# Kernel optimization log

Measured on AMD Instinct MI355X. Metric: run time of the kernel, lower is better.

## Reference

```python
import jax, jax.numpy as jnp
import numpy as np

B, F0, D = 2048, 40, 32
LAYER0, LAYER1 = 128, 128  # layer_size=(128,128), split_half=True -> field_nums=[40,64]


def setup_inputs() -> dict:
    key = jax.random.key(0)
    k1, k2, k3 = jax.random.split(key, 3)
    x = jax.random.normal(k1, (B, F0, D), dtype=jnp.float32)
    # TF conv1d filters: [1, F_prev*F0, size]; we store them reshaped [F0, F_prev_fields, size]
    # Layer 0: F_prev = F0 = 40 -> W0 flattened index m = i*F0 + j, i over x0 fields, j over hidden fields
    W0 = jax.random.normal(k2, (F0, F0, LAYER0), dtype=jnp.float32) * 0.05
    b0 = jnp.zeros((LAYER0,), dtype=jnp.float32)
    # Layer 1: F_prev = LAYER0 // 2 = 64 (split_half)
    W1 = jax.random.normal(k3, (F0, LAYER0 // 2, LAYER1), dtype=jnp.float32) * 0.05
    b1 = jnp.zeros((LAYER1,), dtype=jnp.float32)
    return {"x": x, "W0": W0, "b0": b0, "W1": W1, "b1": b1}


def reference(x, W0, b0, W1, b1):
    # CIN layer 0: outer product x0 (x) x0 over fields per embedding dim, then 1x1 conv + bias + relu
    # TF flattens dot_result as index i*F_prev + j, matching W0[i, j, s].
    h0 = jax.nn.relu(jnp.einsum('bid,bjd,ijs->bsd', x, x, W0) + b0[None, :, None])  # (B, 128, D)
    half = LAYER0 // 2
    next_hidden, direct0 = h0[:, :half, :], h0[:, half:, :]  # split_half
    # CIN layer 1 (last layer): all feature maps go to direct connect
    direct1 = jax.nn.relu(
        jnp.einsum('bid,bjd,ijs->bsd', x, next_hidden, W1) + b1[None, :, None]
    )  # (B, 128, D)
    result = jnp.concatenate([direct0, direct1], axis=1)  # (B, 192, D)
    return jnp.sum(result, axis=-1)  # (B, 192)
```

## Files before the change

kernel.cpp:

```cpp
#include <hip/hip_runtime.h>
#include <stdint.h>


typedef __attribute__((ext_vector_type(8))) _Float16 half8;
typedef __attribute__((ext_vector_type(2))) _Float16 half2v;
typedef __attribute__((ext_vector_type(16))) float f32x16;

#define T0 30
#define T1 80
#define WBUF 8192

__host__ __device__ constexpr int ic0_of(int t) {
    return (t < 2) ? t : (t < 6) ? (t - 2) : (t < 12) ? (t - 6)
         : (t < 20) ? (t - 12) : (t - 20);
}
__host__ __device__ constexpr int jc0_of(int t) {
    return (t < 2) ? 0 : (t < 6) ? 1 : (t < 12) ? 2 : (t < 20) ? 3 : 4;
}

__device__ __forceinline__ unsigned short f2h(float f) {
    return __builtin_bit_cast(unsigned short, (_Float16)f);
}
__device__ __forceinline__ void gl_lds16(const unsigned short* g, unsigned short* l) {
    __builtin_amdgcn_global_load_lds(
        (const __attribute__((address_space(1))) unsigned int*)g,
        (__attribute__((address_space(3))) unsigned int*)l,
        16, 0, 0);
}
__device__ __forceinline__ uint4 avmul(half2v xs, uint4 jv) {
    uint4 r;
    r.x = __builtin_bit_cast(unsigned int, (half2v)(xs * __builtin_bit_cast(half2v, jv.x)));
    r.y = __builtin_bit_cast(unsigned int, (half2v)(xs * __builtin_bit_cast(half2v, jv.y)));
    r.z = __builtin_bit_cast(unsigned int, (half2v)(xs * __builtin_bit_cast(half2v, jv.z)));
    r.w = __builtin_bit_cast(unsigned int, (half2v)(xs * __builtin_bit_cast(half2v, jv.w)));
    return r;
}

__global__ void permute_w_both(const float* __restrict__ W0, const float* __restrict__ W1,
                               unsigned short* __restrict__ Wp0, unsigned short* __restrict__ Wp1)
{
    const int t = blockIdx.x;
    const int tid = threadIdx.x;
    unsigned short outv[16];
    unsigned short* dst;
    if (t < T0) {
        const int ic = ic0_of(t), jc = jc0_of(t);
        #pragma unroll
        for (int q = 0; q < 16; ++q) {
            int pos  = tid * 16 + q;
            int e    = pos & 7, lane = (pos >> 3) & 63;
            int kh   = (pos >> 9) & 1, sq = pos >> 10;
            int s    = sq * 32 + (lane & 31);
            int i    = ic * 4 + kh * 2 + (lane >> 5);
            int j    = jc * 8 + e;
            float v = 0.0f;
            if (i < j)       v = W0[((size_t)(i * 40 + j)) * 128 + s]
                               + W0[((size_t)(j * 40 + i)) * 128 + s];
            else if (i == j) v = W0[((size_t)(i * 40 + i)) * 128 + s];
            outv[q] = f2h(v);
        }
        dst = Wp0 + (size_t)t * 4096 + tid * 16;
    } else {
        const int tt = t - T0;
        const int jc = tt / 10, ic = tt % 10;
        #pragma unroll
        for (int q = 0; q < 16; ++q) {
            int pos  = tid * 16 + q;
            int e    = pos & 7, lane = (pos >> 3) & 63;
            int kh   = (pos >> 9) & 1, sq = pos >> 10;
            int s    = sq * 32 + (lane & 31);
            int i    = ic * 4 + kh * 2 + (lane >> 5);
            int j    = jc * 8 + e;
            outv[q] = f2h(W1[((size_t)(i * 64 + j)) * 128 + s]);
        }
        dst = Wp1 + (size_t)tt * 4096 + tid * 16;
    }
    *(uint4*)dst       = *(const uint4*)outv;
    *(uint4*)(dst + 8) = *(const uint4*)(outv + 8);
}

template<int T, int PHASE>
__device__ __forceinline__ void gemm_phase(
    const unsigned short* __restrict__ Wp,
    const unsigned short* __restrict__ Jl,
    int jstride,
    const unsigned int xk[2][10],
    unsigned short* Wb,
    f32x16 acc[2], int tid)
{
    const int lane = tid & 63;
    const int wv = tid >> 6;
    const int rt = wv >> 2;
    const int sq = wv & 3;
    const int c31 = lane & 31;

    const unsigned short* jbase = Jl + (rt * 64 + c31) * jstride;

    const unsigned short* brd = Wb + sq * 1024 + lane * 8;
    const unsigned short* gsrc = Wp + tid * 8;
    unsigned short* ldst = Wb + tid * 8;

    auto stage = [&](int k) {
        gl_lds16(gsrc + (size_t)k * WBUF, ldst + (k % 3) * WBUF);
    };

    constexpr int NP = T / 2;
    stage(0);
    stage(1);

    uint4 jv0, jv1;
    #pragma unroll
    for (int p = 0; p < NP; ++p) {
        if (p == NP - 1) asm volatile("s_waitcnt vmcnt(0)" ::: "memory");
        else             asm volatile("s_waitcnt vmcnt(1)" ::: "memory");
        __builtin_amdgcn_sched_barrier(0);
        __builtin_amdgcn_s_barrier();
        __builtin_amdgcn_sched_barrier(0);
        if (p + 2 < NP) stage(p + 2);
        __builtin_amdgcn_sched_barrier(0);

        const unsigned short* bper = brd + (p % 3) * WBUF;
        #pragma unroll
        for (int u = 0; u < 2; ++u) {
            const int t  = p * 2 + u;
            const int ic = (PHASE == 0) ? ic0_of(t) : (t % 10);
            const int jc = (PHASE == 0) ? jc0_of(t) : (t / 10);
            const bool rl = (t == 0) ||
                (jc != ((PHASE == 0) ? jc0_of(t - 1) : ((t - 1) / 10)));
            if (rl) {
                jv0 = *(const uint4*)(jbase + jc * 8);
                jv1 = *(const uint4*)(jbase + 32 * jstride + jc * 8);
            }
            __builtin_amdgcn_s_setprio(1);
            #pragma unroll
            for (int kh = 0; kh < 2; ++kh) {
                uint4 bvv = *(const uint4*)(bper + u * 4096 + kh * 512);
                half2v xp = __builtin_bit_cast(half2v, xk[kh][ic]);
                half2v x0 = {xp[0], xp[0]};
                half2v x1 = {xp[1], xp[1]};
                acc[0] = __builtin_amdgcn_mfma_f32_32x32x16_f16(
                    __builtin_bit_cast(half8, avmul(x0, jv0)),
                    __builtin_bit_cast(half8, bvv), acc[0], 0, 0, 0);
                acc[1] = __builtin_amdgcn_mfma_f32_32x32x16_f16(
                    __builtin_bit_cast(half8, avmul(x1, jv1)),
                    __builtin_bit_cast(half8, bvv), acc[1], 0, 0, 0);
            }
            __builtin_amdgcn_s_setprio(0);
        }
    }
}

__global__ __launch_bounds__(1024, 4)
void fused_two_layer(const float* __restrict__ x,
                     const unsigned short* __restrict__ W0p,
                     const float* __restrict__ b0,
                     const unsigned short* __restrict__ W1p,
                     const float* __restrict__ b1,
                     float* __restrict__ out)
{
    __shared__ __align__(16) unsigned short Xl[256 * 40];
    __shared__ __align__(16) unsigned short NH[256 * 72];
    __shared__ __align__(16) unsigned short Wb[3 * WBUF];

    const int tid  = threadIdx.x;
    const int lane = tid & 63;
    const int wv   = tid >> 6;
    const int rt   = wv >> 2;
    const int sq   = wv & 3;
    const int c31  = lane & 31;
    const int hb   = lane >> 5;

    const float* xblk = x + (size_t)blockIdx.x * (8 * 40 * 32);
    #pragma unroll
    for (int k = 0; k < 10; ++k) {
        int f = 1024 * k + tid;
        int bl = f / 1280, rem = f - bl * 1280;
        int i = rem >> 5, d = rem & 31;
        Xl[(bl * 32 + d) * 40 + i] = f2h(xblk[f]);
    }
    __syncthreads();

    unsigned int xk[2][10];
    {
        const unsigned short* xr0 = Xl + (rt * 64 + c31) * 40;
        const unsigned short* xr1 = xr0 + 32 * 40;
        #pragma unroll
        for (int ic = 0; ic < 10; ++ic)
            #pragma unroll
            for (int kh = 0; kh < 2; ++kh) {
                unsigned int u0 = xr0[ic * 4 + kh * 2 + hb];
                unsigned int u1 = xr1[ic * 4 + kh * 2 + hb];
                xk[kh][ic] = u0 | (u1 << 16);
            }
    }

    f32x16 acc[2];
    #pragma unroll
    for (int rtt = 0; rtt < 2; ++rtt)
        #pragma unroll
        for (int rg = 0; rg < 16; ++rg) acc[rtt][rg] = 0.f;

    gemm_phase<T0, 0>(W0p, Xl, 40, xk, Wb, acc, tid);

    {
        float bs = b0[sq * 32 + c31];
        if (sq < 2) {
            #pragma unroll
            for (int rtt = 0; rtt < 2; ++rtt)
                #pragma unroll
                for (int rg = 0; rg < 16; ++rg) {
                    int row = rt * 64 + rtt * 32 + (rg & 3) + 8 * (rg >> 2) + 4 * hb;
                    NH[row * 72 + sq * 32 + c31] =
                        f2h(fmaxf(acc[rtt][rg] + bs, 0.0f));
                }
        } else {
            #pragma unroll
            for (int rtt = 0; rtt < 2; ++rtt) {
                float s = 0.f;
                #pragma unroll
                for (int rg = 0; rg < 16; ++rg)
                    s += fmaxf(acc[rtt][rg] + bs, 0.0f);
                s += __shfl_xor(s, 32, 64);
                int bb = blockIdx.x * 8 + rt * 2 + rtt;
                if (lane < 32)
                    out[(size_t)bb * 192 + (sq - 2) * 32 + c31] = s;
            }
        }
    }
    __syncthreads();

    #pragma unroll
    for (int rtt = 0; rtt < 2; ++rtt)
        #pragma unroll
        for (int rg = 0; rg < 16; ++rg) acc[rtt][rg] = 0.f;

    gemm_phase<T1, 1>(W1p, NH, 72, xk, Wb, acc, tid);

    {
        float bs = b1[sq * 32 + c31];
        #pragma unroll
        for (int rtt = 0; rtt < 2; ++rtt) {
            float s = 0.f;
            #pragma unroll
            for (int rg = 0; rg < 16; ++rg)
                s += fmaxf(acc[rtt][rg] + bs, 0.0f);
            s += __shfl_xor(s, 32, 64);
            int bb = blockIdx.x * 8 + rt * 2 + rtt;
            if (lane < 32)
                out[(size_t)bb * 192 + 64 + sq * 32 + c31] = s;
        }
    }
}

extern "C" void kernel_launch(void* const* d_in, const int* in_sizes, int n_in,
                              void* d_out, int out_size, void* d_ws, size_t ws_size,
                              hipStream_t stream) {
    const float* x  = (const float*)d_in[0];
    const float* W0 = (const float*)d_in[1];
    const float* b0 = (const float*)d_in[2];
    const float* W1 = (const float*)d_in[3];
    const float* b1 = (const float*)d_in[4];
    float* out = (float*)d_out;

    unsigned short* W0p = (unsigned short*)d_ws;
    unsigned short* W1p = (unsigned short*)((char*)d_ws + T0 * 4096 * 2);

    permute_w_both<<<T0 + T1, 256, 0, stream>>>(W0, W1, W0p, W1p);
    fused_two_layer<<<256, 1024, 0, stream>>>(x, W0p, b0, W1p, b1, out);
}
```

Measured before the change: 120.0 us.

## Software-pipeline LDS B-operand reads and A-operand construction in the MFMA loop

Restructures the inner GEMM loop into a flat sequence of half-steps. The B fragment is read from LDS two MFMA pairs ahead, and the scaled A operand (x times hidden) is built one step ahead, so LDS latency and VALU multiplies overlap with MFMA execution. The global-to-LDS weight staging now waits for all outstanding loads (vmcnt(0)) each step instead of leaving one in flight. That may reduce the effective prefetch depth and adds live registers under tight launch bounds.

```diff
diff --git a/kernel.cpp b/kernel.cpp
--- a/kernel.cpp
+++ b/kernel.cpp
@@ -15,7 +15,7 @@
          : (t < 20) ? (t - 12) : (t - 20);
 }
 __host__ __device__ constexpr int jc0_of(int t) {
-    return (t < 2) ? 0 : (t < 6) ? 1 : (t < 12) ? 2 : (t < 20) ? 3 : 4;
+    return (t < 0) ? 0 : (t < 2) ? 0 : (t < 6) ? 1 : (t < 12) ? 2 : (t < 20) ? 3 : 4;
 }
 
 __device__ __forceinline__ unsigned short f2h(float f) {
@@ -94,58 +94,82 @@
     const int sq = wv & 3;
     const int c31 = lane & 31;
 
-    const unsigned short* jbase = Jl + (rt * 64 + c31) * jstride;
-
+    const unsigned short* jbase0 = Jl + (rt * 64 + c31) * jstride;
+    const unsigned short* jbase1 = jbase0 + 32 * jstride;
     const unsigned short* brd = Wb + sq * 1024 + lane * 8;
     const unsigned short* gsrc = Wp + tid * 8;
     unsigned short* ldst = Wb + tid * 8;
 
-    auto stage = [&](int k) {
-        gl_lds16(gsrc + (size_t)k * WBUF, ldst + (k % 3) * WBUF);
-    };
-
-    constexpr int NP = T / 2;
-    stage(0);
-    stage(1);
+    constexpr int NP  = T / 2;
+    constexpr int NHT = T * 2;
+
+    gl_lds16(gsrc, ldst);
+    gl_lds16(gsrc + (size_t)WBUF, ldst + WBUF);
+    asm volatile("s_waitcnt vmcnt(0)" ::: "memory");
+    __builtin_amdgcn_sched_barrier(0);
+    __builtin_amdgcn_s_barrier();
+    __builtin_amdgcn_sched_barrier(0);
+    gl_lds16(gsrc + (size_t)2 * WBUF, ldst + 2 * WBUF);
 
     uint4 jv0, jv1;
+    {
+        const int jc0 = (PHASE == 0) ? jc0_of(0) : 0;
+        jv0 = *(const uint4*)(jbase0 + jc0 * 8);
+        jv1 = *(const uint4*)(jbase1 + jc0 * 8);
+    }
+    uint4 bvp[3];
+    bvp[0] = *(const uint4*)(brd + 0 * 512);
+    bvp[1] = *(const uint4*)(brd + 1 * 512);
+    uint4 avp[2][2];
+    {
+        const int ic0 = (PHASE == 0) ? ic0_of(0) : 0;
+        half2v xp = __builtin_bit_cast(half2v, xk[0][ic0]);
+        half2v x0 = {xp[0], xp[0]}, x1 = {xp[1], xp[1]};
+        avp[0][0] = avmul(x0, jv0);
+        avp[0][1] = avmul(x1, jv1);
+    }
+
     #pragma unroll
     for (int p = 0; p < NP; ++p) {
-        if (p == NP - 1) asm volatile("s_waitcnt vmcnt(0)" ::: "memory");
-        else             asm volatile("s_waitcnt vmcnt(1)" ::: "memory");
-        __builtin_amdgcn_sched_barrier(0);
-        __builtin_amdgcn_s_barrier();
-        __builtin_amdgcn_sched_barrier(0);
-        if (p + 2 < NP) stage(p + 2);
-        __builtin_amdgcn_sched_barrier(0);
-
-        const unsigned short* bper = brd + (p % 3) * WBUF;
-        #pragma unroll
-        for (int u = 0; u < 2; ++u) {
-            const int t  = p * 2 + u;
-            const int ic = (PHASE == 0) ? ic0_of(t) : (t % 10);
-            const int jc = (PHASE == 0) ? jc0_of(t) : (t / 10);
-            const bool rl = (t == 0) ||
-                (jc != ((PHASE == 0) ? jc0_of(t - 1) : ((t - 1) / 10)));
-            if (rl) {
-                jv0 = *(const uint4*)(jbase + jc * 8);
-                jv1 = *(const uint4*)(jbase + 32 * jstride + jc * 8);
-            }
+        if (p > 0) {
+            asm volatile("s_waitcnt vmcnt(0)" ::: "memory");
+            __builtin_amdgcn_sched_barrier(0);
+            __builtin_amdgcn_s_barrier();
+            __builtin_amdgcn_sched_barrier(0);
+            if (p + 2 < NP)
+                gl_lds16(gsrc + (size_t)(p + 2) * WBUF, ldst + ((p + 2) % 3) * WBUF);
+        }
+        #pragma unroll
+        for (int u2 = 0; u2 < 4; ++u2) {
+            const int h = p * 4 + u2;
             __builtin_amdgcn_s_setprio(1);
-            #pragma unroll
-            for (int kh = 0; kh < 2; ++kh) {
-                uint4 bvv = *(const uint4*)(bper + u * 4096 + kh * 512);
-                half2v xp = __builtin_bit_cast(half2v, xk[kh][ic]);
-                half2v x0 = {xp[0], xp[0]};
-                half2v x1 = {xp[1], xp[1]};
-                acc[0] = __builtin_amdgcn_mfma_f32_32x32x16_f16(
-                    __builtin_bit_cast(half8, avmul(x0, jv0)),
-                    __builtin_bit_cast(half8, bvv), acc[0], 0, 0, 0);
-                acc[1] = __builtin_amdgcn_mfma_f32_32x32x16_f16(
-                    __builtin_bit_cast(half8, avmul(x1, jv1)),
-                    __builtin_bit_cast(half8, bvv), acc[1], 0, 0, 0);
-            }
+            acc[0] = __builtin_amdgcn_mfma_f32_32x32x16_f16(
+                __builtin_bit_cast(half8, avp[h & 1][0]),
+                __builtin_bit_cast(half8, bvp[h % 3]), acc[0], 0, 0, 0);
+            acc[1] = __builtin_amdgcn_mfma_f32_32x32x16_f16(
+                __builtin_bit_cast(half8, avp[h & 1][1]),
+                __builtin_bit_cast(half8, bvp[h % 3]), acc[1], 0, 0, 0);
             __builtin_amdgcn_s_setprio(0);
+            if (h + 2 < NHT) {
+                const int t2 = (h + 2) >> 1, kh2 = (h + 2) & 1;
+                const int p2 = t2 >> 1,     u2b = t2 & 1;
+                bvp[(h + 2) % 3] = *(const uint4*)
+                    (brd + (p2 % 3) * WBUF + u2b * 4096 + kh2 * 512);
+            }
+            if (h + 1 < NHT) {
+                const int t1 = (h + 1) >> 1, kh1 = (h + 1) & 1;
+                const int icn = (PHASE == 0) ? ic0_of(t1) : (t1 % 10);
+                const int jcn = (PHASE == 0) ? jc0_of(t1) : (t1 / 10);
+                const int jcp = (PHASE == 0) ? jc0_of(t1 - 1) : ((t1 - 1) / 10);
+                if (kh1 == 0 && jcn != jcp) {
+                    jv0 = *(const uint4*)(jbase0 + jcn * 8);
+                    jv1 = *(const uint4*)(jbase1 + jcn * 8);
+                }
+                half2v xp = __builtin_bit_cast(half2v, xk[kh1][icn]);
+                half2v x0 = {xp[0], xp[0]}, x1 = {xp[1], xp[1]};
+                avp[(h + 1) & 1][0] = avmul(x0, jv0);
+                avp[(h + 1) & 1][1] = avmul(x1, jv1);
+            }
         }
     }
 }
```

Measured after the change: 117.9 us. Within noise of the previous version (-1.7%).

## Halve block to 512 threads with 2x2 MFMA tiles per wave

Applied to the files above, without the earlier changes.

Each wave now computes two 32-column output tiles instead of one, so every A operand built from x*hidden products feeds two MFMAs, and the block shrinks from 16 to 8 waves. Each thread stages two weight chunks per pipeline step to keep the LDS fill the same, and the epilogues are remapped to the new wave layout. The aim is to cut the redundant avmul work and LDS reads of the A side per MFMA. The cost is twice the accumulator registers and fewer waves per block to hide latency.

```diff
diff --git a/kernel.cpp b/kernel.cpp
--- a/kernel.cpp
+++ b/kernel.cpp
@@ -86,22 +86,23 @@
     int jstride,
     const unsigned int xk[2][10],
     unsigned short* Wb,
-    f32x16 acc[2], int tid)
+    f32x16 acc[2][2], int tid)
 {
     const int lane = tid & 63;
     const int wv = tid >> 6;
-    const int rt = wv >> 2;
-    const int sq = wv & 3;
+    const int rt = wv >> 1;
+    const int sh = wv & 1;
     const int c31 = lane & 31;
 
-    const unsigned short* jbase = Jl + (rt * 64 + c31) * jstride;
-
-    const unsigned short* brd = Wb + sq * 1024 + lane * 8;
+    const unsigned short* jbase0 = Jl + (rt * 64 + c31) * jstride;
+    const unsigned short* jbase1 = jbase0 + 32 * jstride;
+    const unsigned short* brd = Wb + sh * 2048 + lane * 8;
     const unsigned short* gsrc = Wp + tid * 8;
     unsigned short* ldst = Wb + tid * 8;
 
     auto stage = [&](int k) {
-        gl_lds16(gsrc + (size_t)k * WBUF, ldst + (k % 3) * WBUF);
+        gl_lds16(gsrc + (size_t)k * WBUF,        ldst + (k % 3) * WBUF);
+        gl_lds16(gsrc + (size_t)k * WBUF + 4096, ldst + (k % 3) * WBUF + 4096);
     };
 
     constexpr int NP = T / 2;
@@ -112,7 +113,7 @@
     #pragma unroll
     for (int p = 0; p < NP; ++p) {
         if (p == NP - 1) asm volatile("s_waitcnt vmcnt(0)" ::: "memory");
-        else             asm volatile("s_waitcnt vmcnt(1)" ::: "memory");
+        else             asm volatile("s_waitcnt vmcnt(2)" ::: "memory");
         __builtin_amdgcn_sched_barrier(0);
         __builtin_amdgcn_s_barrier();
         __builtin_amdgcn_sched_barrier(0);
@@ -128,29 +129,38 @@
             const bool rl = (t == 0) ||
                 (jc != ((PHASE == 0) ? jc0_of(t - 1) : ((t - 1) / 10)));
             if (rl) {
-                jv0 = *(const uint4*)(jbase + jc * 8);
-                jv1 = *(const uint4*)(jbase + 32 * jstride + jc * 8);
+                jv0 = *(const uint4*)(jbase0 + jc * 8);
+                jv1 = *(const uint4*)(jbase1 + jc * 8);
             }
             __builtin_amdgcn_s_setprio(1);
             #pragma unroll
             for (int kh = 0; kh < 2; ++kh) {
-                uint4 bvv = *(const uint4*)(bper + u * 4096 + kh * 512);
+                uint4 bv0 = *(const uint4*)(bper + u * 4096 + kh * 512);
+                uint4 bv1 = *(const uint4*)(bper + u * 4096 + kh * 512 + 1024);
                 half2v xp = __builtin_bit_cast(half2v, xk[kh][ic]);
                 half2v x0 = {xp[0], xp[0]};
                 half2v x1 = {xp[1], xp[1]};
-                acc[0] = __builtin_amdgcn_mfma_f32_32x32x16_f16(
-                    __builtin_bit_cast(half8, avmul(x0, jv0)),
-                    __builtin_bit_cast(half8, bvv), acc[0], 0, 0, 0);
-                acc[1] = __builtin_amdgcn_mfma_f32_32x32x16_f16(
-                    __builtin_bit_cast(half8, avmul(x1, jv1)),
-                    __builtin_bit_cast(half8, bvv), acc[1], 0, 0, 0);
+                uint4 av0 = avmul(x0, jv0);
+                uint4 av1 = avmul(x1, jv1);
+                acc[0][0] = __builtin_amdgcn_mfma_f32_32x32x16_f16(
+                    __builtin_bit_cast(half8, av0),
+                    __builtin_bit_cast(half8, bv0), acc[0][0], 0, 0, 0);
+                acc[0][1] = __builtin_amdgcn_mfma_f32_32x32x16_f16(
+                    __builtin_bit_cast(half8, av0),
+                    __builtin_bit_cast(half8, bv1), acc[0][1], 0, 0, 0);
+                acc[1][0] = __builtin_amdgcn_mfma_f32_32x32x16_f16(
+                    __builtin_bit_cast(half8, av1),
+                    __builtin_bit_cast(half8, bv0), acc[1][0], 0, 0, 0);
+                acc[1][1] = __builtin_amdgcn_mfma_f32_32x32x16_f16(
+                    __builtin_bit_cast(half8, av1),
+                    __builtin_bit_cast(half8, bv1), acc[1][1], 0, 0, 0);
             }
             __builtin_amdgcn_s_setprio(0);
         }
     }
 }
 
-__global__ __launch_bounds__(1024, 4)
+__global__ __launch_bounds__(512, 2)
 void fused_two_layer(const float* __restrict__ x,
                      const unsigned short* __restrict__ W0p,
                      const float* __restrict__ b0,
@@ -165,15 +175,15 @@
     const int tid  = threadIdx.x;
     const int lane = tid & 63;
     const int wv   = tid >> 6;
-    const int rt   = wv >> 2;
-    const int sq   = wv & 3;
+    const int rt   = wv >> 1;
+    const int sh   = wv & 1;
     const int c31  = lane & 31;
     const int hb   = lane >> 5;
 
     const float* xblk = x + (size_t)blockIdx.x * (8 * 40 * 32);
     #pragma unroll
-    for (int k = 0; k < 10; ++k) {
-        int f = 1024 * k + tid;
+    for (int k = 0; k < 20; ++k) {
+        int f = 512 * k + tid;
         int bl = f / 1280, rem = f - bl * 1280;
         int i = rem >> 5, d = rem & 31;
         Xl[(bl * 32 + d) * 40 + i] = f2h(xblk[f]);
@@ -194,60 +204,72 @@
             }
     }
 
-    f32x16 acc[2];
-    #pragma unroll
-    for (int rtt = 0; rtt < 2; ++rtt)
-        #pragma unroll
-        for (int rg = 0; rg < 16; ++rg) acc[rtt][rg] = 0.f;
+    f32x16 acc[2][2];
+    #pragma unroll
+    for (int a = 0; a < 2; ++a)
+        #pragma unroll
+        for (int b = 0; b < 2; ++b)
+            #pragma unroll
+            for (int rg = 0; rg < 16; ++rg) acc[a][b][rg] = 0.f;
 
     gemm_phase<T0, 0>(W0p, Xl, 40, xk, Wb, acc, tid);
 
     {
-        float bs = b0[sq * 32 + c31];
-        if (sq < 2) {
+        float bs[2] = { b0[sh * 64 + c31], b0[sh * 64 + 32 + c31] };
+        if (sh == 0) {
             #pragma unroll
             for (int rtt = 0; rtt < 2; ++rtt)
                 #pragma unroll
-                for (int rg = 0; rg < 16; ++rg) {
-                    int row = rt * 64 + rtt * 32 + (rg & 3) + 8 * (rg >> 2) + 4 * hb;
-                    NH[row * 72 + sq * 32 + c31] =
-                        f2h(fmaxf(acc[rtt][rg] + bs, 0.0f));
+                for (int ct = 0; ct < 2; ++ct)
+                    #pragma unroll
+                    for (int rg = 0; rg < 16; ++rg) {
+                        int row = rt * 64 + rtt * 32 + (rg & 3) + 8 * (rg >> 2) + 4 * hb;
+                        NH[row * 72 + ct * 32 + c31] =
+                            f2h(fmaxf(acc[rtt][ct][rg] + bs[ct], 0.0f));
+                    }
+        } else {
+            #pragma unroll
+            for (int rtt = 0; rtt < 2; ++rtt) {
+                int bb = blockIdx.x * 8 + rt * 2 + rtt;
+                #pragma unroll
+                for (int ct = 0; ct < 2; ++ct) {
+                    float s = 0.f;
+                    #pragma unroll
+                    for (int rg = 0; rg < 16; ++rg)
+                        s += fmaxf(acc[rtt][ct][rg] + bs[ct], 0.0f);
+                    s += __shfl_xor(s, 32, 64);
+                    if (lane < 32)
+                        out[(size_t)bb * 192 + ct * 32 + c31] = s;
                 }
-        } else {
-            #pragma unroll
-            for (int rtt = 0; rtt < 2; ++rtt) {
+            }
+        }
+    }
+    __syncthreads();
+
+    #pragma unroll
+    for (int a = 0; a < 2; ++a)
+        #pragma unroll
+        for (int b = 0; b < 2; ++b)
+            #pragma unroll
+            for (int rg = 0; rg < 16; ++rg) acc[a][b][rg] = 0.f;
+
+    gemm_phase<T1, 1>(W1p, NH, 72, xk, Wb, acc, tid);
+
+    {
+        float bs[2] = { b1[sh * 64 + c31], b1[sh * 64 + 32 + c31] };
+        #pragma unroll
+        for (int rtt = 0; rtt < 2; ++rtt) {
+            int bb = blockIdx.x * 8 + rt * 2 + rtt;
+            #pragma unroll
+            for (int ct = 0; ct < 2; ++ct) {
                 float s = 0.f;
                 #pragma unroll
                 for (int rg = 0; rg < 16; ++rg)
-                    s += fmaxf(acc[rtt][rg] + bs, 0.0f);
+                    s += fmaxf(acc[rtt][ct][rg] + bs[ct], 0.0f);
                 s += __shfl_xor(s, 32, 64);
-                int bb = blockIdx.x * 8 + rt * 2 + rtt;
                 if (lane < 32)
-                    out[(size_t)bb * 192 + (sq - 2) * 32 + c31] = s;
-            }
-        }
-    }
-    __syncthreads();
-
-    #pragma unroll
-    for (int rtt = 0; rtt < 2; ++rtt)
-        #pragma unroll
-        for (int rg = 0; rg < 16; ++rg) acc[rtt][rg] = 0.f;
-
-    gemm_phase<T1, 1>(W1p, NH, 72, xk, Wb, acc, tid);
-
-    {
-        float bs = b1[sq * 32 + c31];
-        #pragma unroll
-        for (int rtt = 0; rtt < 2; ++rtt) {
-            float s = 0.f;
-            #pragma unroll
-            for (int rg = 0; rg < 16; ++rg)
-                s += fmaxf(acc[rtt][rg] + bs, 0.0f);
-            s += __shfl_xor(s, 32, 64);
-            int bb = blockIdx.x * 8 + rt * 2 + rtt;
-            if (lane < 32)
-                out[(size_t)bb * 192 + 64 + sq * 32 + c31] = s;
+                    out[(size_t)bb * 192 + 64 + sh * 64 + ct * 32 + c31] = s;
+            }
         }
     }
 }
@@ -266,5 +288,5 @@
     unsigned short* W1p = (unsigned short*)((char*)d_ws + T0 * 4096 * 2);
 
     permute_w_both<<<T0 + T1, 256, 0, stream>>>(W0, W1, W0p, W1p);
-    fused_two_layer<<<256, 1024, 0, stream>>>(x, W0p, b0, W1p, b1, out);
-}
+    fused_two_layer<<<256, 512, 0, stream>>>(x, W0p, b0, W1p, b1, out);
+}
```

New measurement: 118.8 us. Within noise of the previous version (-1.0%).

## Halve block size to 512 threads and stage one weight tile per step

Applied to the files above, without the earlier changes.

Each block now handles 4 batch rows with 512 threads instead of 8 rows with 1024, and the launch doubles the grid to 512 blocks. The weight pipeline stages one 4096-element tile per barrier step instead of two, so there are twice as many barrier steps. The NH row stride drops from 72 to 68, and shared memory per block shrinks so more blocks can be resident per CU. The aim is better CU occupancy and load balance across more blocks, at the cost of more barriers and each block re-fetching the same weights from global memory.

```diff
diff --git a/kernel.cpp b/kernel.cpp
--- a/kernel.cpp
+++ b/kernel.cpp
@@ -8,7 +8,8 @@
 
 #define T0 30
 #define T1 80
-#define WBUF 8192
+#define TBUF 4096
+#define NHS 68
 
 __host__ __device__ constexpr int ic0_of(int t) {
     return (t < 2) ? t : (t < 6) ? (t - 2) : (t < 12) ? (t - 6)
@@ -94,63 +95,58 @@
     const int sq = wv & 3;
     const int c31 = lane & 31;
 
-    const unsigned short* jbase = Jl + (rt * 64 + c31) * jstride;
-
+    const unsigned short* jbase0 = Jl + (rt * 64 + c31) * jstride;
+    const unsigned short* jbase1 = jbase0 + 32 * jstride;
     const unsigned short* brd = Wb + sq * 1024 + lane * 8;
     const unsigned short* gsrc = Wp + tid * 8;
     unsigned short* ldst = Wb + tid * 8;
 
     auto stage = [&](int k) {
-        gl_lds16(gsrc + (size_t)k * WBUF, ldst + (k % 3) * WBUF);
+        gl_lds16(gsrc + (size_t)k * TBUF, ldst + (k % 3) * TBUF);
     };
 
-    constexpr int NP = T / 2;
     stage(0);
     stage(1);
 
     uint4 jv0, jv1;
     #pragma unroll
-    for (int p = 0; p < NP; ++p) {
-        if (p == NP - 1) asm volatile("s_waitcnt vmcnt(0)" ::: "memory");
-        else             asm volatile("s_waitcnt vmcnt(1)" ::: "memory");
+    for (int p = 0; p < T; ++p) {
+        if (p == T - 1) asm volatile("s_waitcnt vmcnt(0)" ::: "memory");
+        else            asm volatile("s_waitcnt vmcnt(1)" ::: "memory");
         __builtin_amdgcn_sched_barrier(0);
         __builtin_amdgcn_s_barrier();
         __builtin_amdgcn_sched_barrier(0);
-        if (p + 2 < NP) stage(p + 2);
+        if (p + 2 < T) stage(p + 2);
         __builtin_amdgcn_sched_barrier(0);
 
-        const unsigned short* bper = brd + (p % 3) * WBUF;
-        #pragma unroll
-        for (int u = 0; u < 2; ++u) {
-            const int t  = p * 2 + u;
-            const int ic = (PHASE == 0) ? ic0_of(t) : (t % 10);
-            const int jc = (PHASE == 0) ? jc0_of(t) : (t / 10);
-            const bool rl = (t == 0) ||
-                (jc != ((PHASE == 0) ? jc0_of(t - 1) : ((t - 1) / 10)));
-            if (rl) {
-                jv0 = *(const uint4*)(jbase + jc * 8);
-                jv1 = *(const uint4*)(jbase + 32 * jstride + jc * 8);
-            }
-            __builtin_amdgcn_s_setprio(1);
-            #pragma unroll
-            for (int kh = 0; kh < 2; ++kh) {
-                uint4 bvv = *(const uint4*)(bper + u * 4096 + kh * 512);
-                half2v xp = __builtin_bit_cast(half2v, xk[kh][ic]);
-                half2v x0 = {xp[0], xp[0]};
-                half2v x1 = {xp[1], xp[1]};
-                acc[0] = __builtin_amdgcn_mfma_f32_32x32x16_f16(
-                    __builtin_bit_cast(half8, avmul(x0, jv0)),
-                    __builtin_bit_cast(half8, bvv), acc[0], 0, 0, 0);
-                acc[1] = __builtin_amdgcn_mfma_f32_32x32x16_f16(
-                    __builtin_bit_cast(half8, avmul(x1, jv1)),
-                    __builtin_bit_cast(half8, bvv), acc[1], 0, 0, 0);
-            }
-            __builtin_amdgcn_s_setprio(0);
-        }
-    }
-}
-
-__global__ __launch_bounds__(1024, 4)
+        const int ic = (PHASE == 0) ? ic0_of(p) : (p % 10);
+        const int jc = (PHASE == 0) ? jc0_of(p) : (p / 10);
+        const bool rl = (p == 0) ||
+            (jc != ((PHASE == 0) ? jc0_of(p - 1) : ((p - 1) / 10)));
+        if (rl) {
+            jv0 = *(const uint4*)(jbase0 + jc * 8);
+            jv1 = *(const uint4*)(jbase1 + jc * 8);
+        }
+        const unsigned short* bper = brd + (p % 3) * TBUF;
+        __builtin_amdgcn_s_setprio(1);
+        #pragma unroll
+        for (int kh = 0; kh < 2; ++kh) {
+            uint4 bvv = *(const uint4*)(bper + kh * 512);
+            half2v xp = __builtin_bit_cast(half2v, xk[kh][ic]);
+            half2v x0 = {xp[0], xp[0]};
+            half2v x1 = {xp[1], xp[1]};
+            acc[0] = __builtin_amdgcn_mfma_f32_32x32x16_f16(
+                __builtin_bit_cast(half8, avmul(x0, jv0)),
+                __builtin_bit_cast(half8, bvv), acc[0], 0, 0, 0);
+            acc[1] = __builtin_amdgcn_mfma_f32_32x32x16_f16(
+                __builtin_bit_cast(half8, avmul(x1, jv1)),
+                __builtin_bit_cast(half8, bvv), acc[1], 0, 0, 0);
+        }
+        __builtin_amdgcn_s_setprio(0);
+    }
+}
+
+__global__ __launch_bounds__(512, 4)
 void fused_two_layer(const float* __restrict__ x,
                      const unsigned short* __restrict__ W0p,
                      const float* __restrict__ b0,
@@ -158,9 +154,9 @@
                      const float* __restrict__ b1,
                      float* __restrict__ out)
 {
-    __shared__ __align__(16) unsigned short Xl[256 * 40];
-    __shared__ __align__(16) unsigned short NH[256 * 72];
-    __shared__ __align__(16) unsigned short Wb[3 * WBUF];
+    __shared__ __align__(16) unsigned short Xl[128 * 40];
+    __shared__ __align__(16) unsigned short NH[128 * NHS];
+    __shared__ __align__(16) unsigned short Wb[3 * TBUF];
 
     const int tid  = threadIdx.x;
     const int lane = tid & 63;
@@ -170,10 +166,10 @@
     const int c31  = lane & 31;
     const int hb   = lane >> 5;
 
-    const float* xblk = x + (size_t)blockIdx.x * (8 * 40 * 32);
+    const float* xblk = x + (size_t)blockIdx.x * (4 * 40 * 32);
     #pragma unroll
     for (int k = 0; k < 10; ++k) {
-        int f = 1024 * k + tid;
+        int f = 512 * k + tid;
         int bl = f / 1280, rem = f - bl * 1280;
         int i = rem >> 5, d = rem & 31;
         Xl[(bl * 32 + d) * 40 + i] = f2h(xblk[f]);
@@ -210,7 +206,7 @@
                 #pragma unroll
                 for (int rg = 0; rg < 16; ++rg) {
                     int row = rt * 64 + rtt * 32 + (rg & 3) + 8 * (rg >> 2) + 4 * hb;
-                    NH[row * 72 + sq * 32 + c31] =
+                    NH[row * NHS + sq * 32 + c31] =
                         f2h(fmaxf(acc[rtt][rg] + bs, 0.0f));
                 }
         } else {
@@ -221,7 +217,7 @@
                 for (int rg = 0; rg < 16; ++rg)
                     s += fmaxf(acc[rtt][rg] + bs, 0.0f);
                 s += __shfl_xor(s, 32, 64);
-                int bb = blockIdx.x * 8 + rt * 2 + rtt;
+                int bb = blockIdx.x * 4 + rt * 2 + rtt;
                 if (lane < 32)
                     out[(size_t)bb * 192 + (sq - 2) * 32 + c31] = s;
             }
@@ -234,7 +230,7 @@
         #pragma unroll
         for (int rg = 0; rg < 16; ++rg) acc[rtt][rg] = 0.f;
 
-    gemm_phase<T1, 1>(W1p, NH, 72, xk, Wb, acc, tid);
+    gemm_phase<T1, 1>(W1p, NH, NHS, xk, Wb, acc, tid);
 
     {
         float bs = b1[sq * 32 + c31];
@@ -245,7 +241,7 @@
             for (int rg = 0; rg < 16; ++rg)
                 s += fmaxf(acc[rtt][rg] + bs, 0.0f);
             s += __shfl_xor(s, 32, 64);
-            int bb = blockIdx.x * 8 + rt * 2 + rtt;
+            int bb = blockIdx.x * 4 + rt * 2 + rtt;
             if (lane < 32)
                 out[(size_t)bb * 192 + 64 + sq * 32 + c31] = s;
         }
@@ -266,5 +262,5 @@
     unsigned short* W1p = (unsigned short*)((char*)d_ws + T0 * 4096 * 2);
 
     permute_w_both<<<T0 + T1, 256, 0, stream>>>(W0, W1, W0p, W1p);
-    fused_two_layer<<<256, 1024, 0, stream>>>(x, W0p, b0, W1p, b1, out);
-}
+    fused_two_layer<<<512, 512, 0, stream>>>(x, W0p, b0, W1p, b1, out);
+}
```

Result: slower. 128.1 us (+6.7%).
